# Kernel optimization log

Hardware: AMD Instinct MI355X
Metric: run time of the kernel (lower is better)

## Reference

```python
import jax, jax.numpy as jnp
import numpy as np

B, S, T, D, H, HID, V, O = 8, 512, 256, 768, 12, 3072, 50257, 64
HD = D // H  # head dim = 64


def setup_inputs() -> dict:
    key = jax.random.key(0)
    ks = jax.random.split(key, 20)
    s = 0.02
    return {
        'source_input_ids': jax.random.randint(ks[0], (B, S), 0, V, dtype=jnp.int32),
        'encoder_hidden_states': jax.random.normal(ks[1], (B, S, D), dtype=jnp.float32),
        'encoder_attn_mask': jnp.zeros((B, S), dtype=bool),
        'decoder_hidden_states': jax.random.normal(ks[2], (B, T, D), dtype=jnp.float32),
        'onto_ids': jnp.arange(V - O, V, dtype=jnp.int32),
        # MultiheadAttention params (torch layout: W [out,in])
        'Wq': jax.random.normal(ks[3], (D, D)) * s, 'bq': jnp.zeros((D,)),
        'Wk': jax.random.normal(ks[4], (D, D)) * s, 'bk': jnp.zeros((D,)),
        'Wv': jax.random.normal(ks[5], (D, D)) * s, 'bv': jnp.zeros((D,)),
        'Wo': jax.random.normal(ks[6], (D, D)) * s, 'bo': jnp.zeros((D,)),
        # CopyHead: Linear(D, 1)
        'copy_w': jax.random.normal(ks[7], (D, 1)) * s, 'copy_b': jnp.zeros((1,)),
        # Generator FFN: Linear(D, HID) -> relu -> Linear(HID, O)
        'W1': jax.random.normal(ks[8], (HID, D)) * s, 'b1': jnp.zeros((HID,)),
        'W2': jax.random.normal(ks[9], (O, HID)) * s, 'b2': jnp.zeros((O,)),
    }


def _forward(source_input_ids, encoder_hidden_states, encoder_attn_mask,
             decoder_hidden_states, onto_ids, Wq, bq, Wk, bk, Wv, bv, Wo, bo,
             copy_w, copy_b, W1, b1, W2, b2):
    # ---- Generator: FFN + softmax over ontology vocab ----
    h = jax.nn.relu(decoder_hidden_states @ W1.T + b1)
    ontology_probs = jax.nn.softmax(h @ W2.T + b2, axis=-1)  # [B,T,O]

    # ---- MultiheadAttention (batch_first, eval: no dropout) ----
    q = (decoder_hidden_states @ Wq.T + bq).reshape(B, T, H, HD)
    k = (encoder_hidden_states @ Wk.T + bk).reshape(B, S, H, HD)
    v = (encoder_hidden_states @ Wv.T + bv).reshape(B, S, H, HD)
    scores = jnp.einsum('bthd,bshd->bhts', q, k) / jnp.sqrt(jnp.float32(HD))
    scores = jnp.where(encoder_attn_mask[:, None, None, :], -jnp.inf, scores)
    attn = jax.nn.softmax(scores, axis=-1)                       # [B,H,T,S]
    ctx = jnp.einsum('bhts,bshd->bthd', attn, v).reshape(B, T, D)
    context_outputs = ctx @ Wo.T + bo                            # [B,T,D]
    from_source_probs = attn.mean(axis=1)                        # avg heads [B,T,S]

    # ---- CopyHead ----
    copy_probs = jax.nn.sigmoid(context_outputs @ copy_w + copy_b)  # [B,T,1]

    from_source_probs = from_source_probs * copy_probs
    ontology_probs = ontology_probs * (1.0 - copy_probs)

    # ---- scatter-add into full vocab distribution ----
    bi = jnp.arange(B)[:, None, None]
    ti = jnp.arange(T)[None, :, None]
    vocab_probs = jnp.zeros((B, T, V), dtype=copy_probs.dtype)
    vocab_probs = vocab_probs.at[bi, ti, source_input_ids[:, None, :]].add(from_source_probs)
    vocab_probs = vocab_probs.at[bi, ti, onto_ids[None, None, :]].add(ontology_probs)
    return vocab_probs


def reference(source_input_ids, encoder_hidden_states, encoder_attn_mask,
              decoder_hidden_states, onto_ids, Wq, bq, Wk, bk, Wv, bv, Wo, bo,
              copy_w, copy_b, W1, b1, W2, b2):
    return _forward(source_input_ids, encoder_hidden_states, encoder_attn_mask,
                    decoder_hidden_states, onto_ids, Wq, bq, Wk, bk, Wv, bv,
                    Wo, bo, copy_w, copy_b, W1, b1, W2, b2)
```

## Files before the change

kernel.cpp:

```cpp
#include <hip/hip_runtime.h>
#include <hip/hip_bf16.h>
#include <math.h>

constexpr int B = 8, S = 512, T = 256, D = 768, H = 12, HID = 3072;
constexpr int V = 50257, O = 64, HD = 64;

typedef short bf16x8 __attribute__((ext_vector_type(8)));
typedef float f32x4 __attribute__((ext_vector_type(4)));

__device__ __forceinline__ float b2f(unsigned short u) {
  union { float f; unsigned v; } x; x.v = ((unsigned)u) << 16; return x.f;
}
__device__ __forceinline__ unsigned short f2b(float f) {
  __hip_bfloat16 h = __float2bfloat16(f);
  return *(unsigned short*)&h;
}

__device__ __forceinline__ void async16(const void* g, void* l) {
  __builtin_amdgcn_global_load_lds(
      (const __attribute__((address_space(1))) void*)g,
      (__attribute__((address_space(3))) void*)l, 16, 0, 0);
}

constexpr int CH0 = B * T * D / 8;
constexpr int CH1 = CH0 + B * S * D / 8;
constexpr int CH2 = CH1 + HID * D / 8;
constexpr int CH3 = CH2 + D * D / 8;
constexpr int CH4 = CH3 + D * D / 8;
constexpr int CH5 = CH4 + D * D / 8;
constexpr int CH6 = CH5 + O * HID / 8;

__global__ void cvt_all_kernel(
    const float* __restrict__ dec, const float* __restrict__ enc,
    const float* __restrict__ W1, const float* __restrict__ Wq,
    const float* __restrict__ Wk, const float* __restrict__ Wv,
    const float* __restrict__ W2,
    __hip_bfloat16* __restrict__ decb, __hip_bfloat16* __restrict__ encb,
    __hip_bfloat16* __restrict__ WA, __hip_bfloat16* __restrict__ WB,
    __hip_bfloat16* __restrict__ W2b) {
  int i = blockIdx.x * blockDim.x + threadIdx.x;
  const float* src;
  __hip_bfloat16* dst;
  int j;
  if (i < CH0)      { src = dec; dst = decb;                 j = i; }
  else if (i < CH1) { src = enc; dst = encb;                 j = i - CH0; }
  else if (i < CH2) { src = W1;  dst = WA;                   j = i - CH1; }
  else if (i < CH3) { src = Wq;  dst = WA + (size_t)HID * D; j = i - CH2; }
  else if (i < CH4) { src = Wk;  dst = WB;                   j = i - CH3; }
  else if (i < CH5) { src = Wv;  dst = WB + (size_t)D * D;   j = i - CH4; }
  else if (i < CH6) { src = W2;  dst = W2b;                  j = i - CH5; }
  else return;
  size_t e = (size_t)j * 8;
  float4 v0 = *(const float4*)&src[e];
  float4 v1 = *(const float4*)&src[e + 4];
  ushort4 o0, o1;
  o0.x = f2b(v0.x); o0.y = f2b(v0.y); o0.z = f2b(v0.z); o0.w = f2b(v0.w);
  o1.x = f2b(v1.x); o1.y = f2b(v1.y); o1.z = f2b(v1.z); o1.w = f2b(v1.w);
  *(ushort4*)&dst[e] = o0;
  *(ushort4*)&dst[e + 4] = o1;
}

__global__ void weff_kernel(const float* __restrict__ Wo,
                            const float* __restrict__ bo,
                            const float* __restrict__ cw,
                            const float* __restrict__ cb,
                            float* __restrict__ weff) {
  int i = blockIdx.x * blockDim.x + threadIdx.x;
  if (i < D) {
    float acc = 0.f;
    for (int o = 0; o < D; ++o) acc += Wo[(size_t)o * D + i] * cw[o];
    weff[i] = acc;
  } else if (i == D) {
    float acc = cb[0];
    for (int o = 0; o < D; ++o) acc += bo[o] * cw[o];
    weff[D] = acc;
  }
}

template <int BN, int MODE>
__device__ __forceinline__ void gemm_body(
    const __hip_bfloat16* __restrict__ A, const __hip_bfloat16* __restrict__ W,
    const float* __restrict__ bias0, const float* __restrict__ bias1,
    float* __restrict__ Cf, __hip_bfloat16* __restrict__ out0,
    __hip_bfloat16* __restrict__ out1, int M, int N, int K,
    int bx, int by, int kbeg, int kend,
    __hip_bfloat16* Als, __hip_bfloat16* Bls) {
  constexpr int BK = 32;
  constexpr int WTN = BN / 2;
  constexpr int NFRAG = WTN / 16;
  const int tid = threadIdx.x;
  const int lane = tid & 63, wid = tid >> 6;
  const int wm = wid >> 1, wn = wid & 1;
  const int row0 = by * 128, col0 = bx * BN;
  const int lr = lane & 15;
  const int ko = (lane >> 4) * 8;

  f32x4 acc[4][NFRAG] = {};

  for (int k0 = kbeg; k0 < kend; k0 += BK) {
#pragma unroll
    for (int c = 0; c < 2; ++c) {
      int j = tid + c * 256;
      int r = j >> 2, col = (j & 3) * 8;
      async16(&A[(size_t)(row0 + r) * K + k0 + col], (void*)&Als[j * 8]);
    }
#pragma unroll
    for (int c = 0; c < BN / 64; ++c) {
      int j = tid + c * 256;
      int r = j >> 2, col = (j & 3) * 8;
      async16(&W[(size_t)(col0 + r) * K + k0 + col], (void*)&Bls[j * 8]);
    }
    __syncthreads();

    bf16x8 af[4], bfr[NFRAG];
#pragma unroll
    for (int mi = 0; mi < 4; ++mi)
      af[mi] = *(const bf16x8*)&Als[(wm * 64 + mi * 16 + lr) * BK + ko];
#pragma unroll
    for (int ni = 0; ni < NFRAG; ++ni)
      bfr[ni] = *(const bf16x8*)&Bls[(wn * WTN + ni * 16 + lr) * BK + ko];
#pragma unroll
    for (int mi = 0; mi < 4; ++mi)
#pragma unroll
      for (int ni = 0; ni < NFRAG; ++ni)
        acc[mi][ni] = __builtin_amdgcn_mfma_f32_16x16x32_bf16(
            af[mi], bfr[ni], acc[mi][ni], 0, 0, 0);
    __syncthreads();
  }

#pragma unroll
  for (int mi = 0; mi < 4; ++mi) {
    int rbase = row0 + wm * 64 + mi * 16 + (lane >> 4) * 4;
#pragma unroll
    for (int ni = 0; ni < NFRAG; ++ni) {
      int c = col0 + wn * WTN + ni * 16 + lr;
#pragma unroll
      for (int r = 0; r < 4; ++r) {
        int rr = rbase + r;
        float a = acc[mi][ni][r];
        if constexpr (MODE == 1) {
          if (c < HID) {
            out0[(size_t)rr * HID + c] = __float2bfloat16(fmaxf(a + bias0[c], 0.f));
          } else {
            out1[(size_t)rr * D + (c - HID)] = __float2bfloat16(a + bias1[c - HID]);
          }
        } else if constexpr (MODE == 2) {
          if (c < D) {
            out0[(size_t)rr * D + c] = __float2bfloat16(a + bias0[c]);
          } else {
            int d = c - D;
            size_t idx = (((size_t)(rr >> 9) * D + d) << 9) | (size_t)(rr & 511);
            out1[idx] = __float2bfloat16(a + bias1[d]);
          }
        } else {
          Cf[(size_t)rr * N + c] = a;
        }
      }
    }
  }
}

constexpr int KV_BX = (2 * D) / 128;
constexpr int KV_BLOCKS = KV_BX * (B * S / 128);
constexpr int FQ_BX = (HID + D) / 128;
constexpr int FQ_BLOCKS = FQ_BX * (B * T / 128);

__global__ __launch_bounds__(256) void gemm_mega_kernel(
    const __hip_bfloat16* __restrict__ encb, const __hip_bfloat16* __restrict__ WB,
    const float* __restrict__ bk, const float* __restrict__ bv,
    __hip_bfloat16* __restrict__ kb16, __hip_bfloat16* __restrict__ vt,
    const __hip_bfloat16* __restrict__ decb, const __hip_bfloat16* __restrict__ WA,
    const float* __restrict__ b1, const float* __restrict__ bq,
    __hip_bfloat16* __restrict__ hb16, __hip_bfloat16* __restrict__ qb16) {
  __shared__ __hip_bfloat16 Als[128 * 32];
  __shared__ __hip_bfloat16 Bls[128 * 32];
  int bid = blockIdx.x;
  if (bid < KV_BLOCKS) {
    gemm_body<128, 2>(encb, WB, bk, bv, nullptr, kb16, vt,
                      B * S, 2 * D, D, bid % KV_BX, bid / KV_BX, 0, D, Als, Bls);
  } else {
    int r = bid - KV_BLOCKS;
    gemm_body<128, 1>(decb, WA, b1, bq, nullptr, hb16, qb16,
                      B * T, HID + D, D, r % FQ_BX, r / FQ_BX, 0, D, Als, Bls);
  }
}

constexpr int NSPLIT = 16;
constexpr int KCH = HID / NSPLIT;

__global__ __launch_bounds__(256) void gemm_ffn2_kernel(
    const __hip_bfloat16* __restrict__ hb16, const __hip_bfloat16* __restrict__ W2b,
    float* __restrict__ part) {
  __shared__ __hip_bfloat16 Als[128 * 32];
  __shared__ __hip_bfloat16 Bls[64 * 32];
  int sp = blockIdx.x, mt = blockIdx.y;
  gemm_body<64, 3>(hb16, W2b, nullptr, nullptr,
                   part + (size_t)sp * (B * T) * 64, nullptr, nullptr,
                   B * T, 64, HID, 0, mt, sp * KCH, (sp + 1) * KCH, Als, Bls);
}

__global__ void softmax_reduce_kernel(const float* __restrict__ part,
                                      const float* __restrict__ b2v,
                                      float* __restrict__ probs, int rows) {
  int row = blockIdx.x * (blockDim.x >> 6) + (threadIdx.x >> 6);
  int lane = threadIdx.x & 63;
  if (row >= rows) return;
  float x = b2v[lane];
#pragma unroll
  for (int sp = 0; sp < NSPLIT; ++sp)
    x += part[((size_t)sp * rows + row) * 64 + lane];
  float m = x;
#pragma unroll
  for (int o = 32; o > 0; o >>= 1) m = fmaxf(m, __shfl_xor(m, o));
  float e = __expf(x - m);
  float ss = e;
#pragma unroll
  for (int o = 32; o > 0; o >>= 1) ss += __shfl_xor(ss, o);
  probs[(size_t)row * 64 + lane] = e / ss;
}

__global__ __launch_bounds__(256) void attention3_kernel(
    const __hip_bfloat16* __restrict__ q, const __hip_bfloat16* __restrict__ k,
    const __hip_bfloat16* __restrict__ vt, const unsigned char* __restrict__ mask,
    __hip_bfloat16* __restrict__ ctx, __hip_bfloat16* __restrict__ Pg) {
  constexpr int TB = 32;
  constexpr int SCP = 520;
  __shared__ __hip_bfloat16 Qls[TB * 64];
  __shared__ __hip_bfloat16 KVls[128 * 64];
  __shared__ __hip_bfloat16 sc[TB * SCP];
  const int tid = threadIdx.x;
  const int lane = tid & 63, w = tid >> 6;
  const int lr = lane & 15, lg = lane >> 4;
  const int bid = blockIdx.x;
  const int tile = bid & 7;
  const int h = (bid >> 3) % H;
  const int b = bid / (8 * H);
  const int t0 = tile * TB;

  {
    int r = tid >> 3, slot = tid & 7;
    int g = slot ^ (r & 7);
    async16(&q[((size_t)(b * T + t0 + r)) * D + h * 64 + g * 8],
            (void*)&Qls[tid * 8]);
  }

  for (int ch = 0; ch < 4; ++ch) {
    const int s0 = ch * 128;
#pragma unroll
    for (int it = 0; it < 4; ++it) {
      int c = tid + it * 256;
      int r = c >> 3, slot = c & 7;
      int g = slot ^ (r & 7);
      async16(&k[((size_t)(b * S + s0 + r)) * D + h * 64 + g * 8],
              (void*)&KVls[c * 8]);
    }
    __syncthreads();
    f32x4 acc[2][2] = {};
#pragma unroll
    for (int ks = 0; ks < 2; ++ks) {
      bf16x8 af[2], bfr[2];
#pragma unroll
      for (int mi = 0; mi < 2; ++mi) {
        int row = mi * 16 + lr;
        int slot = (4 * ks + lg) ^ (row & 7);
        af[mi] = *(const bf16x8*)&Qls[row * 64 + slot * 8];
      }
#pragma unroll
      for (int ni = 0; ni < 2; ++ni) {
        int row = w * 32 + ni * 16 + lr;
        int slot = (4 * ks + lg) ^ (row & 7);
        bfr[ni] = *(const bf16x8*)&KVls[row * 64 + slot * 8];
      }
#pragma unroll
      for (int mi = 0; mi < 2; ++mi)
#pragma unroll
        for (int ni = 0; ni < 2; ++ni)
          acc[mi][ni] = __builtin_amdgcn_mfma_f32_16x16x32_bf16(
              af[mi], bfr[ni], acc[mi][ni], 0, 0, 0);
    }
#pragma unroll
    for (int ni = 0; ni < 2; ++ni) {
      int s_local = w * 32 + ni * 16 + lr;
      bool msk = mask[b * S + s0 + s_local];
#pragma unroll
      for (int mi = 0; mi < 2; ++mi) {
        int trow = mi * 16 + lg * 4;
#pragma unroll
        for (int rg = 0; rg < 4; ++rg) {
          float val = msk ? -INFINITY : acc[mi][ni][rg] * 0.125f;
          sc[(trow + rg) * SCP + s0 + s_local] = __float2bfloat16(val);
        }
      }
    }
    __syncthreads();
  }

  unsigned short* scu = (unsigned short*)sc;
  unsigned short* pgu = (unsigned short*)Pg;
#pragma unroll
  for (int i = 0; i < 8; ++i) {
    int r = w * 8 + i;
    float x[8];
    float m = -INFINITY;
#pragma unroll
    for (int j = 0; j < 8; ++j) {
      x[j] = b2f(scu[r * SCP + j * 64 + lane]);
      m = fmaxf(m, x[j]);
    }
#pragma unroll
    for (int o = 32; o > 0; o >>= 1) m = fmaxf(m, __shfl_xor(m, o));
    float ssum = 0.f;
#pragma unroll
    for (int j = 0; j < 8; ++j) { x[j] = __expf(x[j] - m); ssum += x[j]; }
#pragma unroll
    for (int o = 32; o > 0; o >>= 1) ssum += __shfl_xor(ssum, o);
    float inv = 1.f / ssum;
#pragma unroll
    for (int j = 0; j < 8; ++j) {
      unsigned short pb = f2b(x[j] * inv);
      scu[r * SCP + j * 64 + lane] = pb;
      pgu[(((size_t)(b * H + h)) * T + t0 + r) * S + j * 64 + lane] = pb;
    }
  }
  __syncthreads();

  f32x4 accp[2] = {};
  for (int ch = 0; ch < 4; ++ch) {
    const int s0 = ch * 128;
#pragma unroll
    for (int it = 0; it < 4; ++it) {
      int c = tid + it * 256;
      int d = c >> 4, slot = c & 15;
      int g = slot ^ (d & 7);
      async16(&vt[(((size_t)(b * H + h)) * 64 + d) * S + s0 + g * 8],
              (void*)&KVls[c * 8]);
    }
    __syncthreads();
#pragma unroll
    for (int ks = 0; ks < 4; ++ks) {
      bf16x8 bfr;
      {
        int brow = w * 16 + lr;
        int slot = (4 * ks + lg) ^ (brow & 7);
        bfr = *(const bf16x8*)&KVls[brow * 128 + slot * 8];
      }
#pragma unroll
      for (int mi = 0; mi < 2; ++mi) {
        int prow = mi * 16 + lr;
        bf16x8 af = *(const bf16x8*)&sc[prow * SCP + s0 + ks * 32 + lg * 8];
        accp[mi] = __builtin_amdgcn_mfma_f32_16x16x32_bf16(af, bfr, accp[mi], 0, 0, 0);
      }
    }
    __syncthreads();
  }
#pragma unroll
  for (int mi = 0; mi < 2; ++mi) {
    int trow = mi * 16 + lg * 4;
#pragma unroll
    for (int rg = 0; rg < 4; ++rg) {
      ctx[((size_t)(b * T + t0 + trow + rg)) * D + h * 64 + w * 16 + lr] =
          __float2bfloat16(accp[mi][rg]);
    }
  }
}

__global__ void copy_head2_kernel(const __hip_bfloat16* __restrict__ ctx,
                                  const float* __restrict__ weff,
                                  float* __restrict__ cpout, int rows) {
  int row = blockIdx.x * (blockDim.x >> 6) + (threadIdx.x >> 6);
  int lane = threadIdx.x & 63;
  if (row >= rows) return;
  const unsigned short* cu = (const unsigned short*)ctx;
  float acc = 0.f;
#pragma unroll
  for (int j = 0; j < D / 64; ++j) {
    int d = j * 64 + lane;
    acc += b2f(cu[(size_t)row * D + d]) * weff[d];
  }
#pragma unroll
  for (int o = 32; o > 0; o >>= 1) acc += __shfl_xor(acc, o);
  if (lane == 0) cpout[row] = 1.f / (1.f + __expf(-(acc + weff[D])));
}

__global__ __launch_bounds__(256) void scatter_fused_kernel(
    const int* __restrict__ src, const int* __restrict__ onto,
    const __hip_bfloat16* __restrict__ Pg, const float* __restrict__ op,
    const float* __restrict__ cp, float* __restrict__ out) {
  const int bt = blockIdx.x;
  const int b = bt >> 8, t = bt & (T - 1);
  const int tid = threadIdx.x;
  float* row = out + (size_t)bt * V;

  uintptr_t addr = (uintptr_t)row;
  int head = (int)(((16 - (addr & 15)) & 15) >> 2);
  if (tid < head) row[tid] = 0.f;
  int n4 = (V - head) >> 2;
  f32x4* row4 = (f32x4*)(row + head);
  const f32x4 z = {0.f, 0.f, 0.f, 0.f};
  for (int i = tid; i < n4; i += 256) row4[i] = z;
  int tail0 = head + (n4 << 2);
  if (tid < V - tail0) row[tail0 + tid] = 0.f;
  __syncthreads();

  const float cpv = cp[bt];
  const unsigned short* pg = (const unsigned short*)Pg;
  for (int s = tid; s < S; s += 256) {
    float sum = 0.f;
#pragma unroll
    for (int h = 0; h < H; ++h)
      sum += b2f(pg[(((size_t)(b * H + h)) * T + t) * S + s]);
    atomicAdd(&row[src[b * S + s]], sum * (1.0f / (float)H) * cpv);
  }
  if (tid < O) {
    atomicAdd(&row[onto[tid]], op[(size_t)bt * O + tid] * (1.f - cpv));
  }
}

extern "C" void kernel_launch(void* const* d_in, const int* in_sizes, int n_in,
                              void* d_out, int out_size, void* d_ws, size_t ws_size,
                              hipStream_t stream) {
  const int* src_ids = (const int*)d_in[0];
  const float* enc = (const float*)d_in[1];
  const unsigned char* mask = (const unsigned char*)d_in[2];
  const float* dec = (const float*)d_in[3];
  const int* onto_ids = (const int*)d_in[4];
  const float* Wq = (const float*)d_in[5];
  const float* bq = (const float*)d_in[6];
  const float* Wk = (const float*)d_in[7];
  const float* bk = (const float*)d_in[8];
  const float* Wv = (const float*)d_in[9];
  const float* bv = (const float*)d_in[10];
  const float* Wo = (const float*)d_in[11];
  const float* bo = (const float*)d_in[12];
  const float* copy_w = (const float*)d_in[13];
  const float* copy_b = (const float*)d_in[14];
  const float* W1 = (const float*)d_in[15];
  const float* b1 = (const float*)d_in[16];
  const float* W2 = (const float*)d_in[17];
  const float* b2 = (const float*)d_in[18];

  const int MT = B * T;
  const int MS = B * S;

  __hip_bfloat16* wb = (__hip_bfloat16*)d_ws;
  __hip_bfloat16* qb16 = wb;    wb += (size_t)MT * D;
  __hip_bfloat16* kb16 = wb;    wb += (size_t)MS * D;
  __hip_bfloat16* vt = wb;      wb += (size_t)MS * D;
  __hip_bfloat16* ctxb16 = wb;  wb += (size_t)MT * D;
  __hip_bfloat16* W2b = wb;     wb += (size_t)O * HID;
  __hip_bfloat16* WB = wb;      wb += (size_t)2 * D * D;
  __hip_bfloat16* WA = wb;      wb += (size_t)(HID + D) * D;
  __hip_bfloat16* Pg = wb;
  __hip_bfloat16* decb = wb;
  __hip_bfloat16* encb = decb + (size_t)MT * D;
  __hip_bfloat16* hb16 = encb + (size_t)MS * D;
  wb += (size_t)B * H * T * S;
  float* wf = (float*)wb;
  float* part = wf;             wf += (size_t)NSPLIT * MT * O;
  float* ontop = wf;            wf += (size_t)MT * O;
  float* cp = wf;               wf += (size_t)MT;
  float* weff = wf;             wf += (size_t)(D + 1);

  float* out = (float*)d_out;

  weff_kernel<<<4, 256, 0, stream>>>(Wo, bo, copy_w, copy_b, weff);

  cvt_all_kernel<<<CH6 / 256, 256, 0, stream>>>(
      dec, enc, W1, Wq, Wk, Wv, W2, decb, encb, WA, WB, W2b);

  gemm_mega_kernel<<<KV_BLOCKS + FQ_BLOCKS, 256, 0, stream>>>(
      encb, WB, bk, bv, kb16, vt, decb, WA, b1, bq, hb16, qb16);

  gemm_ffn2_kernel<<<dim3(NSPLIT, MT / 128), 256, 0, stream>>>(hb16, W2b, part);
  softmax_reduce_kernel<<<MT / 4, 256, 0, stream>>>(part, b2, ontop, MT);

  attention3_kernel<<<B * H * (T / 32), 256, 0, stream>>>(
      qb16, kb16, vt, mask, ctxb16, Pg);

  copy_head2_kernel<<<MT / 4, 256, 0, stream>>>(ctxb16, weff, cp, MT);

  scatter_fused_kernel<<<MT, 256, 0, stream>>>(
      src_ids, onto_ids, Pg, ontop, cp, out);
}
```

Before: 304.4 us.

## Fuse small kernels and move output zeroing into the GEMM launch

The weff computation is folded into the conversion kernel. The softmax-reduce and copy-head kernels are merged into the final scatter kernel. Zeroing the large output buffer moves out of the scatter kernel into extra blocks of the GEMM mega-kernel, which use nontemporal stores so the zeroing can overlap with GEMM work. This cuts launch count and takes the big memset off the scatter's critical path, at the cost of extra per-row reductions inside scatter and bandwidth competition with the GEMMs.

```diff
diff --git a/kernel.cpp b/kernel.cpp
--- a/kernel.cpp
+++ b/kernel.cpp
@@ -30,15 +30,30 @@
 constexpr int CH5 = CH4 + D * D / 8;
 constexpr int CH6 = CH5 + O * HID / 8;
 
-__global__ void cvt_all_kernel(
+__global__ void cvt_weff_kernel(
     const float* __restrict__ dec, const float* __restrict__ enc,
     const float* __restrict__ W1, const float* __restrict__ Wq,
     const float* __restrict__ Wk, const float* __restrict__ Wv,
-    const float* __restrict__ W2,
+    const float* __restrict__ W2, const float* __restrict__ Wo,
+    const float* __restrict__ bo, const float* __restrict__ cw,
+    const float* __restrict__ cb,
     __hip_bfloat16* __restrict__ decb, __hip_bfloat16* __restrict__ encb,
     __hip_bfloat16* __restrict__ WA, __hip_bfloat16* __restrict__ WB,
-    __hip_bfloat16* __restrict__ W2b) {
+    __hip_bfloat16* __restrict__ W2b, float* __restrict__ weff) {
   int i = blockIdx.x * blockDim.x + threadIdx.x;
+  if (i >= CH6) {
+    int j = i - CH6;
+    if (j < D) {
+      float acc = 0.f;
+      for (int o = 0; o < D; ++o) acc += Wo[(size_t)o * D + j] * cw[o];
+      weff[j] = acc;
+    } else if (j == D) {
+      float acc = cb[0];
+      for (int o = 0; o < D; ++o) acc += bo[o] * cw[o];
+      weff[D] = acc;
+    }
+    return;
+  }
   const float* src;
   __hip_bfloat16* dst;
   int j;
@@ -48,8 +63,7 @@
   else if (i < CH3) { src = Wq;  dst = WA + (size_t)HID * D; j = i - CH2; }
   else if (i < CH4) { src = Wk;  dst = WB;                   j = i - CH3; }
   else if (i < CH5) { src = Wv;  dst = WB + (size_t)D * D;   j = i - CH4; }
-  else if (i < CH6) { src = W2;  dst = W2b;                  j = i - CH5; }
-  else return;
+  else              { src = W2;  dst = W2b;                  j = i - CH5; }
   size_t e = (size_t)j * 8;
   float4 v0 = *(const float4*)&src[e];
   float4 v1 = *(const float4*)&src[e + 4];
@@ -58,23 +72,6 @@
   o1.x = f2b(v1.x); o1.y = f2b(v1.y); o1.z = f2b(v1.z); o1.w = f2b(v1.w);
   *(ushort4*)&dst[e] = o0;
   *(ushort4*)&dst[e + 4] = o1;
-}
-
-__global__ void weff_kernel(const float* __restrict__ Wo,
-                            const float* __restrict__ bo,
-                            const float* __restrict__ cw,
-                            const float* __restrict__ cb,
-                            float* __restrict__ weff) {
-  int i = blockIdx.x * blockDim.x + threadIdx.x;
-  if (i < D) {
-    float acc = 0.f;
-    for (int o = 0; o < D; ++o) acc += Wo[(size_t)o * D + i] * cw[o];
-    weff[i] = acc;
-  } else if (i == D) {
-    float acc = cb[0];
-    for (int o = 0; o < D; ++o) acc += bo[o] * cw[o];
-    weff[D] = acc;
-  }
 }
 
 template <int BN, int MODE>
@@ -164,6 +161,9 @@
 constexpr int KV_BLOCKS = KV_BX * (B * S / 128);
 constexpr int FQ_BX = (HID + D) / 128;
 constexpr int FQ_BLOCKS = FQ_BX * (B * T / 128);
+constexpr int GEMM_BLOCKS = KV_BLOCKS + FQ_BLOCKS;
+constexpr int ZERO_BLOCKS = 1184;
+constexpr long long OUT_N4 = (long long)B * T * V / 4;
 
 __global__ __launch_bounds__(256) void gemm_mega_kernel(
     const __hip_bfloat16* __restrict__ encb, const __hip_bfloat16* __restrict__ WB,
@@ -171,17 +171,25 @@
     __hip_bfloat16* __restrict__ kb16, __hip_bfloat16* __restrict__ vt,
     const __hip_bfloat16* __restrict__ decb, const __hip_bfloat16* __restrict__ WA,
     const float* __restrict__ b1, const float* __restrict__ bq,
-    __hip_bfloat16* __restrict__ hb16, __hip_bfloat16* __restrict__ qb16) {
+    __hip_bfloat16* __restrict__ hb16, __hip_bfloat16* __restrict__ qb16,
+    float* __restrict__ out) {
   __shared__ __hip_bfloat16 Als[128 * 32];
   __shared__ __hip_bfloat16 Bls[128 * 32];
   int bid = blockIdx.x;
   if (bid < KV_BLOCKS) {
     gemm_body<128, 2>(encb, WB, bk, bv, nullptr, kb16, vt,
                       B * S, 2 * D, D, bid % KV_BX, bid / KV_BX, 0, D, Als, Bls);
-  } else {
+  } else if (bid < GEMM_BLOCKS) {
     int r = bid - KV_BLOCKS;
     gemm_body<128, 1>(decb, WA, b1, bq, nullptr, hb16, qb16,
                       B * T, HID + D, D, r % FQ_BX, r / FQ_BX, 0, D, Als, Bls);
+  } else {
+    long long zb = bid - GEMM_BLOCKS;
+    f32x4* o4 = (f32x4*)out;
+    const f32x4 z = {0.f, 0.f, 0.f, 0.f};
+    for (long long i = zb * 256 + threadIdx.x; i < OUT_N4;
+         i += (long long)ZERO_BLOCKS * 256)
+      __builtin_nontemporal_store(z, &o4[i]);
   }
 }
 
@@ -197,26 +205,6 @@
   gemm_body<64, 3>(hb16, W2b, nullptr, nullptr,
                    part + (size_t)sp * (B * T) * 64, nullptr, nullptr,
                    B * T, 64, HID, 0, mt, sp * KCH, (sp + 1) * KCH, Als, Bls);
-}
-
-__global__ void softmax_reduce_kernel(const float* __restrict__ part,
-                                      const float* __restrict__ b2v,
-                                      float* __restrict__ probs, int rows) {
-  int row = blockIdx.x * (blockDim.x >> 6) + (threadIdx.x >> 6);
-  int lane = threadIdx.x & 63;
-  if (row >= rows) return;
-  float x = b2v[lane];
-#pragma unroll
-  for (int sp = 0; sp < NSPLIT; ++sp)
-    x += part[((size_t)sp * rows + row) * 64 + lane];
-  float m = x;
-#pragma unroll
-  for (int o = 32; o > 0; o >>= 1) m = fmaxf(m, __shfl_xor(m, o));
-  float e = __expf(x - m);
-  float ss = e;
-#pragma unroll
-  for (int o = 32; o > 0; o >>= 1) ss += __shfl_xor(ss, o);
-  probs[(size_t)row * 64 + lane] = e / ss;
 }
 
 __global__ __launch_bounds__(256) void attention3_kernel(
@@ -364,56 +352,63 @@
   }
 }
 
-__global__ void copy_head2_kernel(const __hip_bfloat16* __restrict__ ctx,
-                                  const float* __restrict__ weff,
-                                  float* __restrict__ cpout, int rows) {
-  int row = blockIdx.x * (blockDim.x >> 6) + (threadIdx.x >> 6);
-  int lane = threadIdx.x & 63;
-  if (row >= rows) return;
-  const unsigned short* cu = (const unsigned short*)ctx;
-  float acc = 0.f;
-#pragma unroll
-  for (int j = 0; j < D / 64; ++j) {
-    int d = j * 64 + lane;
-    acc += b2f(cu[(size_t)row * D + d]) * weff[d];
-  }
-#pragma unroll
-  for (int o = 32; o > 0; o >>= 1) acc += __shfl_xor(acc, o);
-  if (lane == 0) cpout[row] = 1.f / (1.f + __expf(-(acc + weff[D])));
-}
-
-__global__ __launch_bounds__(256) void scatter_fused_kernel(
+__global__ __launch_bounds__(256) void scatter3_kernel(
     const int* __restrict__ src, const int* __restrict__ onto,
-    const __hip_bfloat16* __restrict__ Pg, const float* __restrict__ op,
-    const float* __restrict__ cp, float* __restrict__ out) {
+    const __hip_bfloat16* __restrict__ Pg, const float* __restrict__ part,
+    const float* __restrict__ b2v, const __hip_bfloat16* __restrict__ ctx,
+    const float* __restrict__ weff, float* __restrict__ out) {
   const int bt = blockIdx.x;
   const int b = bt >> 8, t = bt & (T - 1);
   const int tid = threadIdx.x;
+  const int lane = tid & 63;
   float* row = out + (size_t)bt * V;
 
-  uintptr_t addr = (uintptr_t)row;
-  int head = (int)(((16 - (addr & 15)) & 15) >> 2);
-  if (tid < head) row[tid] = 0.f;
-  int n4 = (V - head) >> 2;
-  f32x4* row4 = (f32x4*)(row + head);
-  const f32x4 z = {0.f, 0.f, 0.f, 0.f};
-  for (int i = tid; i < n4; i += 256) row4[i] = z;
-  int tail0 = head + (n4 << 2);
-  if (tid < V - tail0) row[tail0 + tid] = 0.f;
+  __shared__ float red[256];
+  __shared__ float onts[O];
+
+  const unsigned short* cu = (const unsigned short*)ctx + (size_t)bt * D;
+  float a = 0.f;
+#pragma unroll
+  for (int j = 0; j < 3; ++j) {
+    int d = j * 256 + tid;
+    a += b2f(cu[d]) * weff[d];
+  }
+  red[tid] = a;
   __syncthreads();
-
-  const float cpv = cp[bt];
+  for (int st = 128; st > 0; st >>= 1) {
+    if (tid < st) red[tid] += red[tid + st];
+    __syncthreads();
+  }
+  const float cpv = 1.f / (1.f + __expf(-(red[0] + weff[D])));
+  __syncthreads();
+
+  if (tid < 64) {
+    float x = b2v[lane];
+#pragma unroll
+    for (int sp = 0; sp < NSPLIT; ++sp)
+      x += part[((size_t)sp * (B * T) + bt) * 64 + lane];
+    float m = x;
+#pragma unroll
+    for (int o = 32; o > 0; o >>= 1) m = fmaxf(m, __shfl_xor(m, o));
+    float e = __expf(x - m);
+    float ss = e;
+#pragma unroll
+    for (int o = 32; o > 0; o >>= 1) ss += __shfl_xor(ss, o);
+    onts[lane] = e / ss * (1.f - cpv);
+  }
+  __syncthreads();
+
   const unsigned short* pg = (const unsigned short*)Pg;
-  for (int s = tid; s < S; s += 256) {
+#pragma unroll
+  for (int jj = 0; jj < 2; ++jj) {
+    int s = jj * 256 + tid;
     float sum = 0.f;
 #pragma unroll
     for (int h = 0; h < H; ++h)
       sum += b2f(pg[(((size_t)(b * H + h)) * T + t) * S + s]);
     atomicAdd(&row[src[b * S + s]], sum * (1.0f / (float)H) * cpv);
   }
-  if (tid < O) {
-    atomicAdd(&row[onto[tid]], op[(size_t)bt * O + tid] * (1.f - cpv));
-  }
+  if (tid < O) atomicAdd(&row[onto[tid]], onts[tid]);
 }
 
 extern "C" void kernel_launch(void* const* d_in, const int* in_sizes, int n_in,
@@ -457,28 +452,22 @@
   wb += (size_t)B * H * T * S;
   float* wf = (float*)wb;
   float* part = wf;             wf += (size_t)NSPLIT * MT * O;
-  float* ontop = wf;            wf += (size_t)MT * O;
-  float* cp = wf;               wf += (size_t)MT;
   float* weff = wf;             wf += (size_t)(D + 1);
 
   float* out = (float*)d_out;
 
-  weff_kernel<<<4, 256, 0, stream>>>(Wo, bo, copy_w, copy_b, weff);
-
-  cvt_all_kernel<<<CH6 / 256, 256, 0, stream>>>(
-      dec, enc, W1, Wq, Wk, Wv, W2, decb, encb, WA, WB, W2b);
-
-  gemm_mega_kernel<<<KV_BLOCKS + FQ_BLOCKS, 256, 0, stream>>>(
-      encb, WB, bk, bv, kb16, vt, decb, WA, b1, bq, hb16, qb16);
+  cvt_weff_kernel<<<CH6 / 256 + 4, 256, 0, stream>>>(
+      dec, enc, W1, Wq, Wk, Wv, W2, Wo, bo, copy_w, copy_b,
+      decb, encb, WA, WB, W2b, weff);
+
+  gemm_mega_kernel<<<GEMM_BLOCKS + ZERO_BLOCKS, 256, 0, stream>>>(
+      encb, WB, bk, bv, kb16, vt, decb, WA, b1, bq, hb16, qb16, out);
 
   gemm_ffn2_kernel<<<dim3(NSPLIT, MT / 128), 256, 0, stream>>>(hb16, W2b, part);
-  softmax_reduce_kernel<<<MT / 4, 256, 0, stream>>>(part, b2, ontop, MT);
 
   attention3_kernel<<<B * H * (T / 32), 256, 0, stream>>>(
       qb16, kb16, vt, mask, ctxb16, Pg);
 
-  copy_head2_kernel<<<MT / 4, 256, 0, stream>>>(ctxb16, weff, cp, MT);
-
-  scatter_fused_kernel<<<MT, 256, 0, stream>>>(
-      src_ids, onto_ids, Pg, ontop, cp, out);
-}
+  scatter3_kernel<<<MT, 256, 0, stream>>>(
+      src_ids, onto_ids, Pg, part, b2, ctxb16, weff, out);
+}
```

Measured after the change: 281.8 us. 7.4% less time.
